# Kernel optimization log

Measured on AMD Instinct MI355X. Metric: run time of the kernel, lower is better.

## Reference

```python
import jax, jax.numpy as jnp
import numpy as np

B, S, D = 4, 2048, 1024
ATTN_D, OUT_D, H = 1024, 1024, 16
EPS = 1e-12


def setup_inputs() -> dict:
    key = jax.random.key(0)
    ks = jax.random.split(key, 9)
    s = 0.02
    return {
        "x": jax.random.normal(ks[0], (B, S, D), dtype=jnp.float32),
        "wq": jax.random.normal(ks[1], (D, ATTN_D), dtype=jnp.float32) * s,
        "bq": jnp.zeros((ATTN_D,), dtype=jnp.float32),
        "wk": jax.random.normal(ks[2], (D, ATTN_D), dtype=jnp.float32) * s,
        "bk": jnp.zeros((ATTN_D,), dtype=jnp.float32),
        "wv": jax.random.normal(ks[3], (D, ATTN_D), dtype=jnp.float32) * s,
        "bv": jnp.zeros((ATTN_D,), dtype=jnp.float32),
        "wo": jax.random.normal(ks[4], (ATTN_D, OUT_D), dtype=jnp.float32) * s,
        "bo": jnp.zeros((OUT_D,), dtype=jnp.float32),
        "ln_g": jnp.ones((OUT_D,), dtype=jnp.float32),
        "ln_b": jnp.zeros((OUT_D,), dtype=jnp.float32),
    }


def reference(x, wq, bq, wk, bk, wv, bv, wo, bo, ln_g, ln_b):
    b, s, _ = x.shape
    hd = ATTN_D // H  # head_dim
    # projections -> [B, H, S, hd]
    q = (x @ wq + bq).reshape(b, s, H, hd).transpose(0, 2, 1, 3)
    k = (x @ wk + bk).reshape(b, s, H, hd).transpose(0, 2, 1, 3)
    v = (x @ wv + bv).reshape(b, s, H, hd).transpose(0, 2, 1, 3)
    # full O(S^2) score matrix, as in the original module
    scores = jnp.einsum("bhqd,bhkd->bhqk", q, k) / jnp.sqrt(jnp.float32(hd))
    attn = jax.nn.softmax(scores, axis=-1)
    out = jnp.einsum("bhqk,bhkd->bhqd", attn, v)
    out = out.transpose(0, 2, 1, 3).reshape(b, s, ATTN_D)
    out = out @ wo + bo
    # LayerNorm (no residual in this module)
    mu = jnp.mean(out, axis=-1, keepdims=True)
    var = jnp.var(out, axis=-1, keepdims=True)
    out = (out - mu) * jax.lax.rsqrt(var + EPS) * ln_g + ln_b
    return out
```

## Files before the change

kernel.cpp:

```cpp
#include <hip/hip_runtime.h>

typedef __bf16 bf16;
typedef __bf16 bf16x4 __attribute__((ext_vector_type(4)));
typedef __bf16 bf16x8 __attribute__((ext_vector_type(8)));
typedef float f32x4 __attribute__((ext_vector_type(4)));

#define NB 4
#define NS 2048
#define ND 1024
#define NH 16
#define HD 64

#define QSCALE 0.18033688f

__device__ __forceinline__ void gload_lds16(const void* g, void* l) {
  __builtin_amdgcn_global_load_lds(
      (const __attribute__((address_space(1))) void*)g,
      (__attribute__((address_space(3))) void*)l, 16, 0, 0);
}

__device__ __forceinline__ float fast_exp2(float x) {
#if __has_builtin(__builtin_amdgcn_exp2f)
  return __builtin_amdgcn_exp2f(x);
#else
  return exp2f(x);
#endif
}

__global__ __launch_bounds__(256) void k_prep(
    const float* __restrict__ x, bf16* __restrict__ xb,
    const float* __restrict__ wq, const float* __restrict__ wk,
    const float* __restrict__ wv, const float* __restrict__ wo,
    bf16* __restrict__ wqkvT, bf16* __restrict__ woT) {
  __shared__ float t[32][33];
  const int bid = blockIdx.x, tid = threadIdx.x;
  if (bid < 8192) {
    size_t i = ((size_t)bid * 256 + tid) * 4;
    float4 v = *(const float4*)(x + i);
    bf16x4 o = {(__bf16)v.x, (__bf16)v.y, (__bf16)v.z, (__bf16)v.w};
    *(bf16x4*)(xb + i) = o;
    return;
  }
  const int r = bid - 8192;
  const int z = r >> 10;
  const int bx = r & 31, by = (r >> 5) & 31;
  const float* src = z == 0 ? wq : z == 1 ? wk : z == 2 ? wv : wo;
  bf16* dst = z < 3 ? wqkvT + (size_t)z * 1048576 : woT;
  const int tx = tid & 31, ty = tid >> 5;
  const int xx = bx * 32 + tx;
  const int yy = by * 32 + ty;
#pragma unroll
  for (int j = 0; j < 4; ++j)
    t[ty + j * 8][tx] = src[(size_t)(yy + j * 8) * 1024 + xx];
  __syncthreads();
  const int x2 = by * 32 + tx;
  const int y2 = bx * 32 + ty;
#pragma unroll
  for (int j = 0; j < 4; ++j)
    dst[(size_t)(y2 + j * 8) * 1024 + x2] = (__bf16)t[tx][ty + j * 8];
}

__global__ __launch_bounds__(256) void k_vT(const bf16* __restrict__ V,
                                            bf16* __restrict__ Vt) {
  __shared__ bf16 t[64][72];
  int tid = threadIdx.x;
  int bh = blockIdx.x >> 5, st = blockIdx.x & 31;
  int b = bh >> 4, h = bh & 15;
  const bf16* src = V + ((size_t)b * NS + st * 64) * ND + h * HD;
#pragma unroll
  for (int rep = 0; rep < 2; ++rep) {
    int idx = rep * 256 + tid;
    int r = idx >> 3, c8 = (idx & 7) * 8;
    *(bf16x8*)&t[r][c8] = *(const bf16x8*)(src + (size_t)r * ND + c8);
  }
  __syncthreads();
  bf16* dst = Vt + (size_t)bh * HD * NS + st * 64;
#pragma unroll
  for (int rep = 0; rep < 2; ++rep) {
    int idx = rep * 256 + tid;
    int d = idx >> 3, s8 = (idx & 7) * 8;
    bf16x8 v;
#pragma unroll
    for (int j = 0; j < 8; ++j) {
      int jj = (j + tid) & 7;
      v[jj] = t[s8 + jj][d];
    }
    *(bf16x8*)(dst + (size_t)d * NS + s8) = v;
  }
}

__device__ __forceinline__ void gemm256_mainloop(const bf16* __restrict__ A,
                                                 const bf16* __restrict__ BT,
                                                 int bm, int bn, bf16* As,
                                                 bf16* Bs, f32x4 acc[4][4]) {
  const int tid = threadIdx.x;
  const int w = tid >> 6, lane = tid & 63, quad = lane >> 4, l15 = lane & 15;
  const int l7 = l15 & 7, l8 = lane >> 3;
  const int wr = w >> 1, wc = w & 1;
  const int gsw = ((lane & 7) ^ l8) * 8;
  const bf16* gaw = A + (size_t)(bm * 256 + w * 8 + l8) * 1024 + gsw;
  const bf16* gbw = BT + (size_t)(bn * 128 + w * 8 + l8) * 1024 + gsw;
  bf16* daw = As + w * 512;
  bf16* dbw = Bs + w * 512;
  int aoff[4][2], boff[4][2];
#pragma unroll
  for (int mi = 0; mi < 4; ++mi)
#pragma unroll
    for (int ks = 0; ks < 2; ++ks)
      aoff[mi][ks] =
          (wr * 64 + mi * 16 + l15) * 64 + (((ks * 4 + quad) ^ l7) * 8);
#pragma unroll
  for (int ni = 0; ni < 4; ++ni)
#pragma unroll
    for (int ks = 0; ks < 2; ++ks)
      boff[ni][ks] =
          (wc * 64 + ni * 16 + l15) * 64 + (((ks * 4 + quad) ^ l7) * 8);

#pragma unroll
  for (int ri = 0; ri < 4; ++ri)
    gload_lds16(gaw + (size_t)(ri * 64) * 1024, daw + ri * 4096);
#pragma unroll
  for (int ri = 0; ri < 2; ++ri)
    gload_lds16(gbw + (size_t)(ri * 64) * 1024, dbw + ri * 4096);

  for (int kt = 0; kt < 16; ++kt) {
    const int buf = kt & 1;
    __syncthreads();
    if (kt + 1 < 16) {
      const bf16* ga = gaw + (kt + 1) * 64;
      const bf16* gb = gbw + (kt + 1) * 64;
      bf16* da = daw + (buf ^ 1) * 16384;
      bf16* db = dbw + (buf ^ 1) * 8192;
#pragma unroll
      for (int ri = 0; ri < 4; ++ri)
        gload_lds16(ga + (size_t)(ri * 64) * 1024, da + ri * 4096);
#pragma unroll
      for (int ri = 0; ri < 2; ++ri)
        gload_lds16(gb + (size_t)(ri * 64) * 1024, db + ri * 4096);
    }
    const bf16* a_ = As + buf * 16384;
    const bf16* b_ = Bs + buf * 8192;
#pragma unroll
    for (int ks = 0; ks < 2; ++ks) {
      bf16x8 av[4], bv[4];
#pragma unroll
      for (int i = 0; i < 4; ++i)
        av[i] = *(const bf16x8*)(a_ + aoff[i][ks]);
#pragma unroll
      for (int i = 0; i < 4; ++i)
        bv[i] = *(const bf16x8*)(b_ + boff[i][ks]);
#pragma unroll
      for (int mi = 0; mi < 4; ++mi)
#pragma unroll
        for (int ni = 0; ni < 4; ++ni)
          acc[mi][ni] = __builtin_amdgcn_mfma_f32_16x16x32_bf16(
              av[mi], bv[ni], acc[mi][ni], 0, 0, 0);
    }
  }
  __syncthreads();
}

__global__ __launch_bounds__(512, 2) void k_gemm_qkv(
    const bf16* __restrict__ A, const bf16* __restrict__ BT,
    const float* __restrict__ bq, const float* __restrict__ bk,
    const float* __restrict__ bv, bf16* __restrict__ Q, bf16* __restrict__ K,
    bf16* __restrict__ V) {
  __shared__ alignas(16) char smem[98304];
  bf16* As = (bf16*)smem;
  bf16* Bs = (bf16*)(smem + 65536);
  f32x4 acc[4][4] = {};
  const int bm = blockIdx.y, bn = blockIdx.x;
  gemm256_mainloop(A, BT, bm, bn, As, Bs, acc);
  const int tid = threadIdx.x;
  const int w = tid >> 6, lane = tid & 63, quad = lane >> 4, l15 = lane & 15;
  const int wr = w >> 1, wc = w & 1;
  bf16* sEw = (bf16*)smem + w * 4608;
  const int colbase = bn * 128 + wc * 64;
  const int which = colbase >> 10;
  const int nnbase = colbase & 1023;
  const float* bias = which == 0 ? bq : which == 1 ? bk : bv;
  bf16* dst = which == 0 ? Q : which == 1 ? K : V;
  const float scl = which == 0 ? QSCALE : 1.f;
  const int rowbase = bm * 256 + wr * 64;
#pragma unroll
  for (int ni = 0; ni < 4; ++ni) {
    float bb = bias[nnbase + ni * 16 + l15];
#pragma unroll
    for (int mi = 0; mi < 4; ++mi)
#pragma unroll
      for (int r = 0; r < 4; ++r)
        sEw[(mi * 16 + quad * 4 + r) * 72 + ni * 16 + l15] =
            (__bf16)((acc[mi][ni][r] + bb) * scl);
  }
  const int l8 = lane >> 3, g8 = (lane & 7) * 8;
#pragma unroll
  for (int i = 0; i < 8; ++i) {
    int row = i * 8 + l8;
    bf16x8 vv = *(const bf16x8*)(sEw + row * 72 + g8);
    *(bf16x8*)(dst + (size_t)(rowbase + row) * 1024 + nnbase + g8) = vv;
  }
}

__global__ __launch_bounds__(512, 2) void k_gemm_out(
    const bf16* __restrict__ A, const bf16* __restrict__ BT,
    const float* __restrict__ bo, bf16* __restrict__ Yb) {
  __shared__ alignas(16) char smem[98304];
  bf16* As = (bf16*)smem;
  bf16* Bs = (bf16*)(smem + 65536);
  f32x4 acc[4][4] = {};
  const int bm = blockIdx.y, bn = blockIdx.x;
  gemm256_mainloop(A, BT, bm, bn, As, Bs, acc);
  const int tid = threadIdx.x;
  const int w = tid >> 6, lane = tid & 63, quad = lane >> 4, l15 = lane & 15;
  const int wr = w >> 1, wc = w & 1;
  bf16* sEw = (bf16*)smem + w * 4608;
  const int colbase = bn * 128 + wc * 64;
  const int rowbase = bm * 256 + wr * 64;
#pragma unroll
  for (int ni = 0; ni < 4; ++ni) {
    float bb = bo[colbase + ni * 16 + l15];
#pragma unroll
    for (int mi = 0; mi < 4; ++mi)
#pragma unroll
      for (int r = 0; r < 4; ++r)
        sEw[(mi * 16 + quad * 4 + r) * 72 + ni * 16 + l15] =
            (__bf16)(acc[mi][ni][r] + bb);
  }
  const int l8 = lane >> 3, g8 = (lane & 7) * 8;
#pragma unroll
  for (int i = 0; i < 8; ++i) {
    int row = i * 8 + l8;
    bf16x8 vv = *(const bf16x8*)(sEw + row * 72 + g8);
    *(bf16x8*)(Yb + (size_t)(rowbase + row) * 1024 + colbase + g8) = vv;
  }
}

__global__ __launch_bounds__(256, 4) void k_attn(const bf16* __restrict__ Qg,
                                                 const bf16* __restrict__ Kg,
                                                 const bf16* __restrict__ VtG,
                                                 bf16* __restrict__ O) {
  __shared__ alignas(16) char smem[40960];
  bf16* sK = (bf16*)smem;
  bf16* sVt = (bf16*)(smem + 16384);
  const int tid = threadIdx.x;
  const int w = tid >> 6, lane = tid & 63, quad = lane >> 4, l15 = lane & 15;
  const int l7 = l15 & 7, l8 = lane >> 3;
  const int sw = (l15 >> 1) & 3;
  const int bh = blockIdx.x & 63;
  const int qt = blockIdx.x >> 6;
  const int b = bh >> 4, h = bh & 15;
  const bf16* Qh = Qg + (size_t)b * NS * ND + h * HD;
  const bf16* Kh = Kg + (size_t)b * NS * ND + h * HD;
  const bf16* Vh = VtG + (size_t)bh * HD * NS;
  bf16* Pw = (bf16*)(smem + 32768) + w * 1024;

  const int q0 = qt * 128 + w * 32;
  bf16x8 qb[2][2];
#pragma unroll
  for (int ni = 0; ni < 2; ++ni)
#pragma unroll
    for (int ks = 0; ks < 2; ++ks)
      qb[ni][ks] = *(const bf16x8*)(Qh + (size_t)(q0 + ni * 16 + l15) * ND +
                                    ks * 32 + quad * 8);

  const int gsw = ((lane & 7) ^ l8) * 8;
  const bf16* gk = Kh + (size_t)(w * 8 + l8) * ND + gsw;
  const bf16* gv = Vh + (size_t)(w * 8 + l8) * NS + gsw;
  bf16* dk = sK + w * 512;
  bf16* dv = sVt + w * 512;

  f32x4 o_acc[4][2] = {};
  float l_run[2] = {0.f, 0.f};

  int offA[4][2];
#pragma unroll
  for (int mi = 0; mi < 4; ++mi)
#pragma unroll
    for (int ks = 0; ks < 2; ++ks)
      offA[mi][ks] = (mi * 16 + l15) * 64 + (((ks * 4 + quad) ^ l7) * 8);
  int offP[2], wbase[2], wg[2];
#pragma unroll
  for (int ni = 0; ni < 2; ++ni) {
    offP[ni] = (ni * 16 + l15) * 32 + ((quad ^ sw) * 8);
    wbase[ni] = (ni * 16 + l15) * 32 + (quad & 1) * 4;
  }
#pragma unroll
  for (int m2 = 0; m2 < 2; ++m2)
    wg[m2] = (((m2 * 2 + (quad >> 1)) ^ sw) * 8);

  gload_lds16(gk, dk);
  gload_lds16(gk + 32 * ND, dk + 2048);
  gload_lds16(gv, dv);
  gload_lds16(gv + 32 * NS, dv + 2048);

  for (int it = 0; it < NS / 64; ++it) {
    const int buf = (it & 1) * 4096;
    __syncthreads();
    if (it + 1 < NS / 64) {
      const int nbuf = 4096 - buf;
      const bf16* gk1 = gk + (size_t)(it + 1) * 64 * ND;
      const bf16* gv1 = gv + (it + 1) * 64;
      gload_lds16(gk1, dk + nbuf);
      gload_lds16(gk1 + 32 * ND, dk + nbuf + 2048);
      gload_lds16(gv1, dv + nbuf);
      gload_lds16(gv1 + 32 * NS, dv + nbuf + 2048);
    }

#pragma unroll
    for (int hf = 0; hf < 2; ++hf) {
#pragma unroll
      for (int m2 = 0; m2 < 2; ++m2) {
        const int mi = 2 * hf + m2;
        f32x4 s[2] = {};
#pragma unroll
        for (int ks = 0; ks < 2; ++ks) {
          bf16x8 ak = *(const bf16x8*)(sK + buf + offA[mi][ks]);
#pragma unroll
          for (int ni = 0; ni < 2; ++ni)
            s[ni] = __builtin_amdgcn_mfma_f32_16x16x32_bf16(ak, qb[ni][ks],
                                                            s[ni], 0, 0, 0);
        }
#pragma unroll
        for (int ni = 0; ni < 2; ++ni) {
#pragma unroll
          for (int r = 0; r < 4; ++r) {
            s[ni][r] = fast_exp2(s[ni][r]);
            l_run[ni] += s[ni][r];
          }
          bf16x4 p = {(__bf16)s[ni][0], (__bf16)s[ni][1], (__bf16)s[ni][2],
                      (__bf16)s[ni][3]};
          *(bf16x4*)(Pw + wbase[ni] + wg[m2]) = p;
        }
      }

      bf16x8 pb[2];
#pragma unroll
      for (int ni = 0; ni < 2; ++ni)
        pb[ni] = *(const bf16x8*)(Pw + offP[ni]);
#pragma unroll
      for (int mi = 0; mi < 4; ++mi) {
        bf16x8 av = *(const bf16x8*)(sVt + buf + offA[mi][hf]);
#pragma unroll
        for (int ni = 0; ni < 2; ++ni)
          o_acc[mi][ni] = __builtin_amdgcn_mfma_f32_16x16x32_bf16(
              av, pb[ni], o_acc[mi][ni], 0, 0, 0);
      }
    }
  }

#pragma unroll
  for (int ni = 0; ni < 2; ++ni) {
    float l = l_run[ni];
    l += __shfl_xor(l, 16, 64);
    l += __shfl_xor(l, 32, 64);
    float inv = 1.f / l;
    int q = q0 + ni * 16 + l15;
    size_t orow = ((size_t)b * NS + q) * 1024 + h * 64;
#pragma unroll
    for (int mi = 0; mi < 4; ++mi) {
      bf16x4 ov = {
          (__bf16)(o_acc[mi][ni][0] * inv), (__bf16)(o_acc[mi][ni][1] * inv),
          (__bf16)(o_acc[mi][ni][2] * inv), (__bf16)(o_acc[mi][ni][3] * inv)};
      *(bf16x4*)(O + orow + mi * 16 + quad * 4) = ov;
    }
  }
}

__global__ __launch_bounds__(256) void k_ln(const bf16* __restrict__ Yb,
                                            const float* __restrict__ g,
                                            const float* __restrict__ bta,
                                            float* __restrict__ out) {
  int row = blockIdx.x, tid = threadIdx.x;
  bf16x4 vb = *(const bf16x4*)(Yb + (size_t)row * 1024 + tid * 4);
  float4 v = {(float)vb[0], (float)vb[1], (float)vb[2], (float)vb[3]};
  float sm = v.x + v.y + v.z + v.w;
  float sq = v.x * v.x + v.y * v.y + v.z * v.z + v.w * v.w;
#pragma unroll
  for (int off = 1; off < 64; off <<= 1) {
    sm += __shfl_xor(sm, off, 64);
    sq += __shfl_xor(sq, off, 64);
  }
  __shared__ float red[8];
  int w = tid >> 6, lane = tid & 63;
  if (lane == 0) {
    red[w] = sm;
    red[4 + w] = sq;
  }
  __syncthreads();
  sm = red[0] + red[1] + red[2] + red[3];
  sq = red[4] + red[5] + red[6] + red[7];
  float mu = sm * (1.f / 1024.f);
  float var = sq * (1.f / 1024.f) - mu * mu;
  float rstd = rsqrtf(var + 1e-12f);
  float4 g4 = ((const float4*)g)[tid];
  float4 b4 = ((const float4*)bta)[tid];
  float4 o;
  o.x = (v.x - mu) * rstd * g4.x + b4.x;
  o.y = (v.y - mu) * rstd * g4.y + b4.y;
  o.z = (v.z - mu) * rstd * g4.z + b4.z;
  o.w = (v.w - mu) * rstd * g4.w + b4.w;
  ((float4*)(out + (size_t)row * 1024))[tid] = o;
}

extern "C" void kernel_launch(void* const* d_in, const int* in_sizes, int n_in,
                              void* d_out, int out_size, void* d_ws,
                              size_t ws_size, hipStream_t stream) {
  const float* x = (const float*)d_in[0];
  const float* wq = (const float*)d_in[1];
  const float* bq = (const float*)d_in[2];
  const float* wk = (const float*)d_in[3];
  const float* bk = (const float*)d_in[4];
  const float* wv = (const float*)d_in[5];
  const float* bv = (const float*)d_in[6];
  const float* wo = (const float*)d_in[7];
  const float* bo = (const float*)d_in[8];
  const float* ln_g = (const float*)d_in[9];
  const float* ln_b = (const float*)d_in[10];
  float* out = (float*)d_out;

  char* ws = (char*)d_ws;
  bf16* xb = (bf16*)ws;          ws += 16777216;
  bf16* wqkvT = (bf16*)ws;       ws += 6291456;
  bf16* woT = (bf16*)ws;         ws += 2097152;
  bf16* Qh = (bf16*)ws;          ws += 16777216;
  bf16* Kh = (bf16*)ws;          ws += 16777216;
  bf16* Vh = (bf16*)ws;          ws += 16777216;
  bf16* Vt = (bf16*)ws;          ws += 16777216;
  bf16* AOb = (bf16*)ws;         ws += 16777216;
  bf16* Yb = (bf16*)ws;          ws += 16777216;

  k_prep<<<12288, 256, 0, stream>>>(x, xb, wq, wk, wv, wo, wqkvT, woT);

  k_gemm_qkv<<<dim3(24, 32), 512, 0, stream>>>(xb, wqkvT, bq, bk, bv, Qh, Kh,
                                               Vh);
  k_vT<<<NB * NH * 32, 256, 0, stream>>>(Vh, Vt);
  k_attn<<<NB * NH * (NS / 128), 256, 0, stream>>>(Qh, Kh, Vt, AOb);
  k_gemm_out<<<dim3(8, 32), 512, 0, stream>>>(AOb, woT, bo, Yb);
  k_ln<<<8192, 256, 0, stream>>>(Yb, ln_g, ln_b, out);
}
```

Measured before the change: 287.0 us.

## Fuse output projection GEMM with LayerNorm using full-row 32x1024 tiles

Replaces the 256x128-tiled output GEMM plus separate LayerNorm kernel with one kernel in which each block computes a 32-row by 1024-column strip, so row statistics are reduced in-block and normalized fp32 output is written directly. This removes the bf16 Yb intermediate round trip and one launch, and it also drops the bf16 rounding of the pre-norm values. In exchange, each block streams the full 1024x1024 weight through LDS with only 32 rows of A, so weight reuse per load drops sharply. The grid also shrinks to 256 blocks of 512 threads using about 132 KB of LDS each, which limits occupancy to one block per CU.

```diff
diff --git a/kernel.cpp b/kernel.cpp
--- a/kernel.cpp
+++ b/kernel.cpp
@@ -201,37 +201,146 @@
   }
 }
 
-__global__ __launch_bounds__(512, 2) void k_gemm_out(
+__global__ __launch_bounds__(512) void k_gemm_out_ln(
     const bf16* __restrict__ A, const bf16* __restrict__ BT,
-    const float* __restrict__ bo, bf16* __restrict__ Yb) {
-  __shared__ alignas(16) char smem[98304];
+    const float* __restrict__ bo, const float* __restrict__ g,
+    const float* __restrict__ beta, float* __restrict__ out) {
+  __shared__ alignas(16) char smem[135168];
   bf16* As = (bf16*)smem;
-  bf16* Bs = (bf16*)(smem + 65536);
-  f32x4 acc[4][4] = {};
-  const int bm = blockIdx.y, bn = blockIdx.x;
-  gemm256_mainloop(A, BT, bm, bn, As, Bs, acc);
+  bf16* Bs = (bf16*)(smem + 4096);
   const int tid = threadIdx.x;
   const int w = tid >> 6, lane = tid & 63, quad = lane >> 4, l15 = lane & 15;
-  const int wr = w >> 1, wc = w & 1;
-  bf16* sEw = (bf16*)smem + w * 4608;
-  const int colbase = bn * 128 + wc * 64;
-  const int rowbase = bm * 256 + wr * 64;
-#pragma unroll
-  for (int ni = 0; ni < 4; ++ni) {
-    float bb = bo[colbase + ni * 16 + l15];
-#pragma unroll
-    for (int mi = 0; mi < 4; ++mi)
-#pragma unroll
-      for (int r = 0; r < 4; ++r)
-        sEw[(mi * 16 + quad * 4 + r) * 72 + ni * 16 + l15] =
-            (__bf16)(acc[mi][ni][r] + bb);
-  }
-  const int l8 = lane >> 3, g8 = (lane & 7) * 8;
-#pragma unroll
-  for (int i = 0; i < 8; ++i) {
-    int row = i * 8 + l8;
-    bf16x8 vv = *(const bf16x8*)(sEw + row * 72 + g8);
-    *(bf16x8*)(Yb + (size_t)(rowbase + row) * 1024 + colbase + g8) = vv;
+  const int lrow = lane >> 2, lcol = (lane & 3) * 8;
+  const int rowbase = blockIdx.x * 32;
+
+  f32x4 acc[2][8] = {};
+
+  auto stage = [&](int kt, int slot) {
+#pragma unroll
+    for (int i = 0; i < 8; ++i) {
+      const int r0 = (w * 8 + i) * 16;
+      gload_lds16(BT + (size_t)(r0 + lrow) * 1024 + kt * 32 + lcol,
+                  Bs + slot * 32768 + r0 * 32);
+    }
+    if (w < 2)
+      gload_lds16(A + (size_t)(rowbase + w * 16 + lrow) * 1024 + kt * 32 +
+                      lcol,
+                  As + slot * 1024 + w * 512);
+  };
+
+  stage(0, 0);
+  for (int kt = 0; kt < 32; ++kt) {
+    const int buf = kt & 1;
+    __syncthreads();
+    if (kt + 1 < 32) stage(kt + 1, buf ^ 1);
+    const bf16* a_ = As + buf * 1024;
+    const bf16* b_ = Bs + buf * 32768;
+    bf16x8 av[2], bv[8];
+#pragma unroll
+    for (int mi = 0; mi < 2; ++mi)
+      av[mi] = *(const bf16x8*)(a_ + (mi * 16 + l15) * 32 + quad * 8);
+#pragma unroll
+    for (int ni = 0; ni < 8; ++ni)
+      bv[ni] =
+          *(const bf16x8*)(b_ + (size_t)(w * 128 + ni * 16 + l15) * 32 +
+                           quad * 8);
+#pragma unroll
+    for (int mi = 0; mi < 2; ++mi)
+#pragma unroll
+      for (int ni = 0; ni < 8; ++ni)
+        acc[mi][ni] = __builtin_amdgcn_mfma_f32_16x16x32_bf16(
+            av[mi], bv[ni], acc[mi][ni], 0, 0, 0);
+  }
+  __syncthreads();
+
+  float* redS = (float*)smem;
+  float* redQ = (float*)(smem + 1024);
+  float* mustd = (float*)(smem + 2048);
+
+  float bb[8];
+#pragma unroll
+  for (int ni = 0; ni < 8; ++ni) bb[ni] = bo[w * 128 + ni * 16 + l15];
+#pragma unroll
+  for (int mi = 0; mi < 2; ++mi)
+#pragma unroll
+    for (int ni = 0; ni < 8; ++ni)
+#pragma unroll
+      for (int r = 0; r < 4; ++r) acc[mi][ni][r] += bb[ni];
+
+#pragma unroll
+  for (int mi = 0; mi < 2; ++mi)
+#pragma unroll
+    for (int r = 0; r < 4; ++r) {
+      float sm = 0.f, sq = 0.f;
+#pragma unroll
+      for (int ni = 0; ni < 8; ++ni) {
+        float v = acc[mi][ni][r];
+        sm += v;
+        sq += v * v;
+      }
+#pragma unroll
+      for (int off = 1; off < 16; off <<= 1) {
+        sm += __shfl_xor(sm, off, 64);
+        sq += __shfl_xor(sq, off, 64);
+      }
+      if (l15 == 0) {
+        int row = mi * 16 + quad * 4 + r;
+        redS[w * 32 + row] = sm;
+        redQ[w * 32 + row] = sq;
+      }
+    }
+  __syncthreads();
+  if (tid < 32) {
+    float sm = 0.f, sq = 0.f;
+#pragma unroll
+    for (int ww = 0; ww < 8; ++ww) {
+      sm += redS[ww * 32 + tid];
+      sq += redQ[ww * 32 + tid];
+    }
+    float mu = sm * (1.f / 1024.f);
+    float var = sq * (1.f / 1024.f) - mu * mu;
+    mustd[tid * 2] = mu;
+    mustd[tid * 2 + 1] = rsqrtf(var + 1e-12f);
+  }
+  __syncthreads();
+
+  float gg[8], be[8];
+#pragma unroll
+  for (int ni = 0; ni < 8; ++ni) {
+    gg[ni] = g[w * 128 + ni * 16 + l15];
+    be[ni] = beta[w * 128 + ni * 16 + l15];
+  }
+  float mur[2][4], rsr[2][4];
+#pragma unroll
+  for (int mi = 0; mi < 2; ++mi)
+#pragma unroll
+    for (int r = 0; r < 4; ++r) {
+      int row = mi * 16 + quad * 4 + r;
+      mur[mi][r] = mustd[row * 2];
+      rsr[mi][r] = mustd[row * 2 + 1];
+    }
+
+  float* sEw = (float*)(smem + 4096) + w * 2176;
+  const int l4 = lane >> 4, c4 = (lane & 15) * 4;
+#pragma unroll
+  for (int hf = 0; hf < 2; ++hf) {
+#pragma unroll
+    for (int mi = 0; mi < 2; ++mi)
+#pragma unroll
+      for (int nj = 0; nj < 4; ++nj) {
+        const int ni = hf * 4 + nj;
+#pragma unroll
+        for (int r = 0; r < 4; ++r)
+          sEw[(mi * 16 + quad * 4 + r) * 68 + nj * 16 + l15] =
+              (acc[mi][ni][r] - mur[mi][r]) * rsr[mi][r] * gg[ni] + be[ni];
+      }
+#pragma unroll
+    for (int i = 0; i < 8; ++i) {
+      int row = i * 4 + l4;
+      float4 v = *(const float4*)(sEw + row * 68 + c4);
+      *(float4*)(out + (size_t)(rowbase + row) * 1024 + w * 128 + hf * 64 +
+                 c4) = v;
+    }
   }
 }
 
@@ -366,42 +475,6 @@
   }
 }
 
-__global__ __launch_bounds__(256) void k_ln(const bf16* __restrict__ Yb,
-                                            const float* __restrict__ g,
-                                            const float* __restrict__ bta,
-                                            float* __restrict__ out) {
-  int row = blockIdx.x, tid = threadIdx.x;
-  bf16x4 vb = *(const bf16x4*)(Yb + (size_t)row * 1024 + tid * 4);
-  float4 v = {(float)vb[0], (float)vb[1], (float)vb[2], (float)vb[3]};
-  float sm = v.x + v.y + v.z + v.w;
-  float sq = v.x * v.x + v.y * v.y + v.z * v.z + v.w * v.w;
-#pragma unroll
-  for (int off = 1; off < 64; off <<= 1) {
-    sm += __shfl_xor(sm, off, 64);
-    sq += __shfl_xor(sq, off, 64);
-  }
-  __shared__ float red[8];
-  int w = tid >> 6, lane = tid & 63;
-  if (lane == 0) {
-    red[w] = sm;
-    red[4 + w] = sq;
-  }
-  __syncthreads();
-  sm = red[0] + red[1] + red[2] + red[3];
-  sq = red[4] + red[5] + red[6] + red[7];
-  float mu = sm * (1.f / 1024.f);
-  float var = sq * (1.f / 1024.f) - mu * mu;
-  float rstd = rsqrtf(var + 1e-12f);
-  float4 g4 = ((const float4*)g)[tid];
-  float4 b4 = ((const float4*)bta)[tid];
-  float4 o;
-  o.x = (v.x - mu) * rstd * g4.x + b4.x;
-  o.y = (v.y - mu) * rstd * g4.y + b4.y;
-  o.z = (v.z - mu) * rstd * g4.z + b4.z;
-  o.w = (v.w - mu) * rstd * g4.w + b4.w;
-  ((float4*)(out + (size_t)row * 1024))[tid] = o;
-}
-
 extern "C" void kernel_launch(void* const* d_in, const int* in_sizes, int n_in,
                               void* d_out, int out_size, void* d_ws,
                               size_t ws_size, hipStream_t stream) {
@@ -427,7 +500,6 @@
   bf16* Vh = (bf16*)ws;          ws += 16777216;
   bf16* Vt = (bf16*)ws;          ws += 16777216;
   bf16* AOb = (bf16*)ws;         ws += 16777216;
-  bf16* Yb = (bf16*)ws;          ws += 16777216;
 
   k_prep<<<12288, 256, 0, stream>>>(x, xb, wq, wk, wv, wo, wqkvT, woT);
 
@@ -435,6 +507,5 @@
                                                Vh);
   k_vT<<<NB * NH * 32, 256, 0, stream>>>(Vh, Vt);
   k_attn<<<NB * NH * (NS / 128), 256, 0, stream>>>(Qh, Kh, Vt, AOb);
-  k_gemm_out<<<dim3(8, 32), 512, 0, stream>>>(AOb, woT, bo, Yb);
-  k_ln<<<8192, 256, 0, stream>>>(Yb, ln_g, ln_b, out);
-}
+  k_gemm_out_ln<<<256, 512, 0, stream>>>(AOb, woT, bo, ln_g, ln_b, out);
+}
```

Result: slower. 298.0 us (+3.9%).
